# Kernel tuning notes

Measured on AMD Instinct MI355X. Metric: run time of the kernel, lower is better.

## Reference

```python
import jax, jax.numpy as jnp
import numpy as np

B, F, T, V, L, ATTR, E, H = 256, 2048, 40, 10000, 20, 400, 512, 1024
A = E            # attention_dim = embedding_dim
D1 = H + F + E   # lstm1 input dim
D2 = H + F       # lstm2 input dim


def setup_inputs() -> dict:
    key = jax.random.key(0)
    ks = jax.random.split(key, 16)
    def rn(k, shape, s=0.02):
        return jax.random.normal(k, shape, jnp.float32) * s
    return dict(
        input_feats=jax.random.normal(ks[0], (B, F, T), jnp.float32),
        input_atts=jax.random.uniform(ks[1], (B, ATTR), jnp.float32),
        input_sents=jax.random.randint(ks[2], (B, L), 0, V),
        attr_W=rn(ks[3], (D2, ATTR)), attr_b=jnp.zeros((D2,), jnp.float32),
        emb=rn(ks[4], (V, E)),
        l1_Wih=rn(ks[5], (4 * H, D1)), l1_Whh=rn(ks[6], (4 * H, H)),
        l1_bih=jnp.zeros((4 * H,), jnp.float32), l1_bhh=jnp.zeros((4 * H,), jnp.float32),
        l2_Wih=rn(ks[7], (4 * H, D2)), l2_Whh=rn(ks[8], (4 * H, H)),
        l2_bih=jnp.zeros((4 * H,), jnp.float32), l2_bhh=jnp.zeros((4 * H,), jnp.float32),
        prob_W=rn(ks[9], (V, H)), prob_b=jnp.zeros((V,), jnp.float32),
        attf_W=rn(ks[10], (A, F)), attf_b=jnp.zeros((A,), jnp.float32),
        atth_W=rn(ks[11], (A, H)), atth_b=jnp.zeros((A,), jnp.float32),
        atta_W=rn(ks[12], (1, A)), atta_b=jnp.zeros((1,), jnp.float32),
    )


def lstm_cell(x, h, c, Wih, Whh, bih, bhh):
    # torch.nn.LSTMCell gate order: i, f, g, o
    g = x @ Wih.T + bih + h @ Whh.T + bhh
    i, f, gg, o = jnp.split(g, 4, axis=1)
    c_new = jax.nn.sigmoid(f) * c + jax.nn.sigmoid(i) * jnp.tanh(gg)
    h_new = jax.nn.sigmoid(o) * jnp.tanh(c_new)
    return h_new, c_new


def reference(input_feats, input_atts, input_sents, attr_W, attr_b, emb,
              l1_Wih, l1_Whh, l1_bih, l1_bhh, l2_Wih, l2_Whh, l2_bih, l2_bhh,
              prob_W, prob_b, attf_W, attf_b, atth_W, atth_b, atta_W, atta_b):
    mean_feature = input_feats.mean(axis=2)                       # [B,F]
    # attention_linear_f(features) is timestep-independent: precompute once
    embed_f = jnp.einsum('bft,af->bta', input_feats, attf_W) + attf_b  # [B,T,A]

    zeros = jnp.zeros((B, H), jnp.float32)
    h1, c1 = zeros, zeros
    # lstm2 primed with embedded attributes
    attr_vec = input_atts @ attr_W.T + attr_b                     # [B,D2]
    h2, c2 = lstm_cell(attr_vec, zeros, zeros, l2_Wih, l2_Whh, l2_bih, l2_bhh)

    word_vecs = emb[input_sents[:, :L - 1]]                       # [B,L-1,E] teacher forcing

    def step(carry, wv):
        h1, c1, h2, c2 = carry
        x1 = jnp.concatenate([h2, mean_feature, wv], axis=1)      # [B,D1]
        h1, c1 = lstm_cell(x1, h1, c1, l1_Wih, l1_Whh, l1_bih, l1_bhh)
        # soft attention over T feature slots
        eh = h1 @ atth_W.T + atth_b                               # [B,A]
        scores = jnp.tanh(embed_f + eh[:, None, :]) @ atta_W[0] + atta_b[0]  # [B,T]
        alpha = jax.nn.softmax(scores, axis=1)                    # [B,T]
        v_hat = jnp.einsum('bt,bft->bf', alpha, input_feats)      # [B,F]
        x2 = jnp.concatenate([h1, v_hat], axis=1)                 # [B,D2]
        h2, c2 = lstm_cell(x2, h2, c2, l2_Wih, l2_Whh, l2_bih, l2_bhh)
        predict = h2 @ prob_W.T + prob_b                          # [B,V]
        gen_word = jnp.argmax(predict, axis=1)                    # argmax(log_softmax) == argmax(logits)
        return (h1, c1, h2, c2), (gen_word, predict)

    _, (gens, preds) = jax.lax.scan(step, (h1, c1, h2, c2),
                                    jnp.swapaxes(word_vecs, 0, 1))
    outputs = gens.T                                              # [B,L-1]
    output_preds = jnp.swapaxes(preds, 0, 1)                      # [B,L-1,V]
    return outputs, output_preds
```

## Files before the change

kernel.cpp:

```cpp
#include <hip/hip_runtime.h>
#include <cmath>

#define B_ 256
#define F_ 2048
#define T_ 40
#define V_ 10000
#define L_ 20
#define ATTR_ 400
#define E_ 512
#define H_ 1024
#define A_ 512
#define NS_ 19

typedef float f32x4 __attribute__((ext_vector_type(4)));
typedef short bf16x8 __attribute__((ext_vector_type(8)));

__device__ __forceinline__ float sigm(float x) { return 1.0f / (1.0f + expf(-x)); }

__device__ __forceinline__ unsigned short f2bf(float x) {
    unsigned int u = __float_as_uint(x);
    u += 0x7fffu + ((u >> 16) & 1u);
    return (unsigned short)(u >> 16);
}
__device__ __forceinline__ float bf2f(unsigned short h) {
    return __uint_as_float(((unsigned int)h) << 16);
}
__device__ __forceinline__ void gload16(const void* g, void* l) {
    __builtin_amdgcn_global_load_lds(
        (const __attribute__((address_space(1))) unsigned int*)g,
        (__attribute__((address_space(3))) unsigned int*)l, 16, 0, 0);
}
__device__ __forceinline__ f32x4 mfma16(bf16x8 a, bf16x8 b, f32x4 c) {
    return __builtin_amdgcn_mfma_f32_16x16x32_bf16(a, b, c, 0, 0, 0);
}
__device__ __forceinline__ long swz(int m, int k, int mslabs) {
    return ((long)(k >> 5) * mslabs + (m >> 4)) * 512
         + ((k >> 3) & 3) * 128 + (m & 15) * 8 + (k & 7);
}

struct GChunk {
    const unsigned short* Ahi; const unsigned short* Alo;
    const unsigned short* Bhi; const unsigned short* Blo;
    long ask, bsk;
    int kc;
};
struct GChunks { GChunk c[8]; };

template<int DIRECT>
__global__ __launch_bounds__(512) void gemm_mfma(
    GChunks ch, float* __restrict__ out, const float* __restrict__ bias,
    int Mreal, long ldc, long zstride)
{
    const GChunk cc = ch.c[blockIdx.z];
    const int tid  = threadIdx.x;
    const int lane = tid & 63;
    const int w    = tid >> 6;
    const int m0   = blockIdx.x * 128;
    const int n0   = blockIdx.y * 256;

    __shared__ __align__(16) unsigned short lds[3][48][512];

    const unsigned short* gp[6];
    long adv[6];
#pragma unroll
    for (int q = 0; q < 6; ++q) {
        int s = w * 6 + q;
        const unsigned short* base; long off;
        if (s < 16) {
            base = (s & 8) ? cc.Alo : cc.Ahi;
            off = ((long)(m0 >> 4) + (s & 7)) * 512;
            adv[q] = cc.ask;
        } else {
            int t2 = s - 16;
            base = (t2 & 16) ? cc.Blo : cc.Bhi;
            off = ((long)(n0 >> 4) + (t2 & 15)) * 512;
            adv[q] = cc.bsk;
        }
        gp[q] = base + off + lane * 8;
    }

    auto stage = [&](int t) {
#pragma unroll
        for (int q = 0; q < 6; ++q) {
            gload16(gp[q], &lds[t][w * 6 + q][lane * 8]);
            gp[q] += adv[q];
        }
    };

    f32x4 zero4 = {0.f, 0.f, 0.f, 0.f};
    f32x4 acc[4][4];
#pragma unroll
    for (int i = 0; i < 4; ++i)
#pragma unroll
        for (int j = 0; j < 4; ++j) acc[i][j] = zero4;

    const int ms0 = (w >> 2) * 4;
    const int ns0 = (w & 3) * 4;

    const int kst = cc.kc >> 5;
    stage(0);
    if (kst > 1) stage(1);
    for (int ks = 0; ks < kst; ++ks) {
        if (ks + 1 < kst) asm volatile("s_waitcnt vmcnt(6)" ::: "memory");
        else              asm volatile("s_waitcnt vmcnt(0)" ::: "memory");
        __builtin_amdgcn_s_barrier();
        __builtin_amdgcn_sched_barrier(0);
        if (ks + 2 < kst) stage((ks + 2) % 3);
        const unsigned short (*buf)[512] = lds[ks % 3];
        bf16x8 ah[4], al[4], bh[4], bl[4];
#pragma unroll
        for (int i = 0; i < 4; ++i) {
            ah[i] = *(const bf16x8*)&buf[ms0 + i][lane * 8];
            al[i] = *(const bf16x8*)&buf[8 + ms0 + i][lane * 8];
            bh[i] = *(const bf16x8*)&buf[16 + ns0 + i][lane * 8];
            bl[i] = *(const bf16x8*)&buf[32 + ns0 + i][lane * 8];
        }
#pragma unroll
        for (int i = 0; i < 4; ++i)
#pragma unroll
            for (int j = 0; j < 4; ++j) {
                acc[i][j] = mfma16(ah[i], bh[j], acc[i][j]);
                acc[i][j] = mfma16(ah[i], bl[j], acc[i][j]);
                acc[i][j] = mfma16(al[i], bh[j], acc[i][j]);
            }
    }

    const int wm = (w >> 2) * 64;
    const int wn = (w & 3) * 64;
    const int mr = (lane >> 4) * 4;
    const int ncl = lane & 15;
    float* P = DIRECT ? out : out + (long)blockIdx.z * zstride;
#pragma unroll
    for (int i = 0; i < 4; ++i) {
        int mm = m0 + wm + i * 16 + mr;
        if (mm < Mreal) {
            float4 bv = {0.f, 0.f, 0.f, 0.f};
            if (DIRECT && bias) bv = *(const float4*)&bias[mm];
#pragma unroll
            for (int j = 0; j < 4; ++j) {
                int bb = n0 + wn + j * 16 + ncl;
                float4 v;
                v.x = acc[i][j].x + bv.x;
                v.y = acc[i][j].y + bv.y;
                v.z = acc[i][j].z + bv.z;
                v.w = acc[i][j].w + bv.w;
                *(float4*)&P[(long)bb * ldc + mm] = v;
            }
        }
    }
}

__global__ __launch_bounds__(256) void lstm_fused(
    const float* __restrict__ P, int nz, long zstride,
    const float* __restrict__ base, int bmode,
    float* __restrict__ c,
    unsigned short* __restrict__ hhi, unsigned short* __restrict__ hlo)
{
    int idx = blockIdx.x * 256 + threadIdx.x;
    int n = idx & 1023;
    int b = idx >> 10;
    long r = (long)b * 4096 + n;
    float ig = 0.f, fg = 0.f, gg = 0.f, og = 0.f;
    for (int z = 0; z < nz; ++z) {
        const float* p = P + (long)z * zstride + r;
        ig += p[0]; fg += p[1024]; gg += p[2048]; og += p[3072];
    }
    if (bmode == 1) {
        const float* q = base + r;
        ig += q[0]; fg += q[1024]; gg += q[2048]; og += q[3072];
    } else {
        ig += base[n]; fg += base[1024 + n]; gg += base[2048 + n]; og += base[3072 + n];
    }
    float cn = sigm(fg) * c[idx] + sigm(ig) * tanhf(gg);
    c[idx] = cn;
    float hv = sigm(og) * tanhf(cn);
    unsigned short hi = f2bf(hv);
    long o = swz(b, n, 16);
    hhi[o] = hi;
    hlo[o] = f2bf(hv - bf2f(hi));
}

__global__ __launch_bounds__(256) void attention_kernel(
    const float* __restrict__ ef, const float* __restrict__ Pe,
    const float* __restrict__ feats, const float* __restrict__ atta_W,
    const float* __restrict__ atta_b,
    unsigned short* __restrict__ vhhi, unsigned short* __restrict__ vhlo)
{
    __shared__ float eh_s[512], aw_s[512], sc_s[48];
    int b = blockIdx.x, tid = threadIdx.x;
    float e0 = 0.f, e1 = 0.f;
#pragma unroll
    for (int z = 0; z < 8; ++z) {
        const float* p = Pe + (long)z * (512 * 256) + b * 512;
        e0 += p[tid]; e1 += p[tid + 256];
    }
    eh_s[tid] = e0; eh_s[tid + 256] = e1;
    aw_s[tid] = atta_W[tid]; aw_s[tid + 256] = atta_W[tid + 256];
    __syncthreads();
    int w = tid >> 6, lane = tid & 63;
    float ab0 = atta_b[0];
    for (int i = 0; i < 10; ++i) {
        int t = w * 10 + i;
        const float* ep = ef + ((long)b * T_ + t) * A_ + lane * 8;
        float4 e1v = *(const float4*)ep;
        float4 e2v = *(const float4*)(ep + 4);
        int a = lane * 8;
        float s = tanhf(e1v.x + eh_s[a+0]) * aw_s[a+0] + tanhf(e1v.y + eh_s[a+1]) * aw_s[a+1]
                + tanhf(e1v.z + eh_s[a+2]) * aw_s[a+2] + tanhf(e1v.w + eh_s[a+3]) * aw_s[a+3]
                + tanhf(e2v.x + eh_s[a+4]) * aw_s[a+4] + tanhf(e2v.y + eh_s[a+5]) * aw_s[a+5]
                + tanhf(e2v.z + eh_s[a+6]) * aw_s[a+6] + tanhf(e2v.w + eh_s[a+7]) * aw_s[a+7];
#pragma unroll
        for (int o = 32; o > 0; o >>= 1) s += __shfl_down(s, o, 64);
        if (lane == 0) sc_s[t] = s + ab0;
    }
    __syncthreads();
    if (tid < 64) {
        float v = (tid < T_) ? sc_s[tid] : -INFINITY;
        float m = v;
#pragma unroll
        for (int o = 32; o > 0; o >>= 1) m = fmaxf(m, __shfl_down(m, o, 64));
        m = __shfl(m, 0, 64);
        float e = (tid < T_) ? expf(v - m) : 0.f;
        float su = e;
#pragma unroll
        for (int o = 32; o > 0; o >>= 1) su += __shfl_down(su, o, 64);
        su = __shfl(su, 0, 64);
        if (tid < T_) sc_s[tid] = e / su;
    }
    __syncthreads();
    for (int cc = 0; cc < 8; ++cc) {
        int f = cc * 256 + tid;
        const float* fp = feats + ((long)b * F_ + f) * T_;
        float acc = 0.f;
#pragma unroll
        for (int t4 = 0; t4 < 10; ++t4) {
            float4 v = *(const float4*)(fp + t4 * 4);
            acc += sc_s[t4*4+0] * v.x + sc_s[t4*4+1] * v.y
                 + sc_s[t4*4+2] * v.z + sc_s[t4*4+3] * v.w;
        }
        unsigned short hi = f2bf(acc);
        long o = swz(b, f, 16);
        vhhi[o] = hi;
        vhlo[o] = f2bf(acc - bf2f(hi));
    }
}

__global__ void reduce_rows(float* __restrict__ out, const float* __restrict__ P,
                            const float* __restrict__ base, int S, long zstride,
                            int n, int mask)
{
    long e = ((long)blockIdx.x * 256 + threadIdx.x) * 4;
    if (e >= n) return;
    float4 s = *(const float4*)&P[e];
    for (int z = 1; z < S; ++z) {
        float4 p = *(const float4*)&P[(long)z * zstride + e];
        s.x += p.x; s.y += p.y; s.z += p.z; s.w += p.w;
    }
    if (base) {
        float4 bv = *(const float4*)&base[e & mask];
        s.x += bv.x; s.y += bv.y; s.z += bv.z; s.w += bv.w;
    }
    *(float4*)&out[e] = s;
}

__global__ void cast_swz(const float* __restrict__ src,
    unsigned short* __restrict__ dhi, unsigned short* __restrict__ dlo,
    long srcld, int nrows, int ncols, int mslabs)
{
    long g = (long)blockIdx.x * 256 + threadIdx.x;
    int within = (int)(g & 511);
    long slab = g >> 9;
    int kblk = (int)(slab / mslabs);
    int ms = (int)(slab - (long)kblk * mslabs);
    int kg = within >> 7, r = (within >> 3) & 15, j = within & 7;
    int m = ms * 16 + r;
    int k = kblk * 32 + kg * 8 + j;
    float v = (m < nrows && k < ncols) ? src[(long)m * srcld + k] : 0.f;
    unsigned short hi = f2bf(v);
    dhi[g] = hi; dlo[g] = f2bf(v - bf2f(hi));
}

__global__ void mean_cast(const float* __restrict__ feats,
                          unsigned short* __restrict__ mh, unsigned short* __restrict__ ml)
{
    int idx = blockIdx.x * 256 + threadIdx.x;
    const float* p = feats + (long)idx * T_;
    float s = 0.f;
#pragma unroll
    for (int t = 0; t < T_; t += 4) {
        float4 v = *(const float4*)(p + t);
        s += v.x + v.y + v.z + v.w;
    }
    s *= (1.0f / (float)T_);
    unsigned short hi = f2bf(s);
    int b = idx >> 11, f = idx & 2047;
    long o = swz(b, f, 16);
    mh[o] = hi; ml[o] = f2bf(s - bf2f(hi));
}

__global__ __launch_bounds__(256) void transpose_cast_feats(
    const float* __restrict__ feats,
    unsigned short* __restrict__ fh, unsigned short* __restrict__ fl)
{
    __shared__ float tf[2560];
    int b = blockIdx.y, f0 = blockIdx.x * 64;
    const float* src = feats + (long)b * (F_ * T_) + (long)f0 * T_;
#pragma unroll
    for (int q = 0; q < 10; ++q) tf[q * 256 + threadIdx.x] = src[q * 256 + threadIdx.x];
    __syncthreads();
#pragma unroll
    for (int q = 0; q < 10; ++q) {
        int idx = q * 256 + threadIdx.x;
        int t = idx >> 6, fo = idx & 63;
        int f = f0 + fo;
        int bt = b * T_ + t;
        float v = tf[fo * 40 + t];
        unsigned short hi = f2bf(v);
        long o = ((long)(f >> 5) * 640 + (bt >> 4)) * 512
               + ((f >> 3) & 3) * 128 + (bt & 15) * 8 + (f & 7);
        fh[o] = hi; fl[o] = f2bf(v - bf2f(hi));
    }
}

__global__ void wv_gather_cast(const int* __restrict__ sents, const float* __restrict__ emb,
    unsigned short* __restrict__ wh, unsigned short* __restrict__ wl, int s)
{
    int idx = blockIdx.x * 256 + threadIdx.x;
    int b = idx >> 9, e = idx & 511;
    int wd = sents[b * L_ + s];
    float v = emb[(long)wd * E_ + e];
    unsigned short hi = f2bf(v);
    long o = swz(b, e, 16);
    wh[o] = hi; wl[o] = f2bf(v - bf2f(hi));
}

__global__ void vec_add_kernel(const float* a, const float* b, float* out, int n)
{
    int i = blockIdx.x * 256 + threadIdx.x;
    if (i < n) out[i] = a[i] + b[i];
}

__global__ __launch_bounds__(256) void argmax_kernel(
    const float* __restrict__ dout_preds, float* __restrict__ outw, int s)
{
    __shared__ float sv[256];
    __shared__ int   si[256];
    int b = blockIdx.x, tid = threadIdx.x;
    const float* row = dout_preds + (long)b * (NS_ * (long)V_) + (long)s * V_;
    float best = -INFINITY; int bi = 0x7fffffff;
    for (int v = tid; v < V_; v += 256) {
        float x = row[v];
        if (x > best) { best = x; bi = v; }
    }
    sv[tid] = best; si[tid] = bi;
    __syncthreads();
    for (int o = 128; o > 0; o >>= 1) {
        if (tid < o) {
            float ov = sv[tid + o]; int oi = si[tid + o];
            if (ov > sv[tid] || (ov == sv[tid] && oi < si[tid])) { sv[tid] = ov; si[tid] = oi; }
        }
        __syncthreads();
    }
    if (tid == 0) outw[b * NS_ + s] = (float)si[0];
}

extern "C" void kernel_launch(void* const* d_in, const int* in_sizes, int n_in,
                              void* d_out, int out_size, void* d_ws, size_t ws_size,
                              hipStream_t stream)
{
    (void)in_sizes; (void)n_in; (void)out_size; (void)ws_size;
    const float* feats  = (const float*)d_in[0];
    const float* atts   = (const float*)d_in[1];
    const int*   sents  = (const int*)d_in[2];
    const float* attr_W = (const float*)d_in[3];
    const float* attr_b = (const float*)d_in[4];
    const float* emb    = (const float*)d_in[5];
    const float* l1_Wih = (const float*)d_in[6];
    const float* l1_Whh = (const float*)d_in[7];
    const float* l1_bih = (const float*)d_in[8];
    const float* l1_bhh = (const float*)d_in[9];
    const float* l2_Wih = (const float*)d_in[10];
    const float* l2_Whh = (const float*)d_in[11];
    const float* l2_bih = (const float*)d_in[12];
    const float* l2_bhh = (const float*)d_in[13];
    const float* prob_W = (const float*)d_in[14];
    const float* prob_b = (const float*)d_in[15];
    const float* attf_W = (const float*)d_in[16];
    const float* attf_b = (const float*)d_in[17];
    const float* atth_W = (const float*)d_in[18];
    const float* atth_b = (const float*)d_in[19];
    const float* atta_W = (const float*)d_in[20];
    const float* atta_b = (const float*)d_in[21];

    float* out = (float*)d_out;
    float* preds = out + B_ * NS_;

    char* pp = (char*)d_ws;
    auto alloc = [&](size_t n) { char* r = pp; pp += (n + 255) & ~(size_t)255; return r; };

    const long AS256 = 256L * 512;
    const long AS632 = 632L * 512;
    const long AS32  = 32L * 512;
    const long AS192 = 192L * 512;
    const long BS    = 16L * 512;
    const long BS640 = 640L * 512;

    char* R = alloc(83886080UL);
    unsigned short* fTh   = (unsigned short*)R;
    unsigned short* fTl   = (unsigned short*)(R + 41943040UL);
    unsigned short* W2ihh = (unsigned short*)R;
    unsigned short* W2ihl = (unsigned short*)(R + 25165824UL);
    unsigned short* Wmh   = (unsigned short*)(R + 50331648UL);
    unsigned short* Wml   = (unsigned short*)(R + 67108864UL);

    unsigned short* W1ah  = (unsigned short*)alloc(8388608);
    unsigned short* W1al  = (unsigned short*)alloc(8388608);
    unsigned short* W1wh  = (unsigned short*)alloc(4194304);
    unsigned short* W1wl  = (unsigned short*)alloc(4194304);
    unsigned short* W1hhh = (unsigned short*)alloc(8388608);
    unsigned short* W1hhl = (unsigned short*)alloc(8388608);
    unsigned short* W2hhh = (unsigned short*)alloc(8388608);
    unsigned short* W2hhl = (unsigned short*)alloc(8388608);
    unsigned short* Wprh  = (unsigned short*)alloc(20709376);
    unsigned short* Wprl  = (unsigned short*)alloc(20709376);
    unsigned short* Wahh  = (unsigned short*)alloc(1048576);
    unsigned short* Wahl  = (unsigned short*)alloc(1048576);
    unsigned short* Wafh  = (unsigned short*)alloc(2097152);
    unsigned short* Wafl  = (unsigned short*)alloc(2097152);
    unsigned short* Warh  = (unsigned short*)alloc(2555904);
    unsigned short* Warl  = (unsigned short*)alloc(2555904);

    float* ef    = (float*)alloc(10240L*512*4);
    float* base1 = (float*)alloc(4096L*256*4);
    float* Pbuf  = (float*)alloc(7L*4096*256*4);
    float* attrv = Pbuf;

    unsigned short* h1h = (unsigned short*)alloc(524288);
    unsigned short* h1l = (unsigned short*)alloc(524288);
    unsigned short* h2h = (unsigned short*)alloc(524288);
    unsigned short* h2l = (unsigned short*)alloc(524288);
    unsigned short* wvh = (unsigned short*)alloc(262144);
    unsigned short* wvl = (unsigned short*)alloc(262144);
    unsigned short* vhh = (unsigned short*)alloc(1048576);
    unsigned short* vhl = (unsigned short*)alloc(1048576);
    unsigned short* mfh = (unsigned short*)alloc(1048576);
    unsigned short* mfl = (unsigned short*)alloc(1048576);
    unsigned short* attsh = (unsigned short*)alloc(212992);
    unsigned short* attsl = (unsigned short*)alloc(212992);
    unsigned short* avh = (unsigned short*)alloc(1572864);
    unsigned short* avl = (unsigned short*)alloc(1572864);
    float* c1 = (float*)alloc(256L*1024*4);
    float* c2 = (float*)alloc(256L*1024*4);
    float* bihbhh1 = (float*)alloc(4096*4);
    float* bias2   = (float*)alloc(4096*4);
    float* efbias  = (float*)alloc(512*4);

    hipMemsetAsync(c1, 0, 256L*1024*4, stream);
    hipMemsetAsync(c2, 0, 256L*1024*4, stream);
    hipMemsetAsync(h1h, 0, 524288, stream);
    hipMemsetAsync(h1l, 0, 524288, stream);

    vec_add_kernel<<<16, 256, 0, stream>>>(l1_bih, l1_bhh, bihbhh1, 4096);
    vec_add_kernel<<<16, 256, 0, stream>>>(l2_bih, l2_bhh, bias2, 4096);
    vec_add_kernel<<<2, 256, 0, stream>>>(attf_b, atth_b, efbias, 512);
    mean_cast<<<2048, 256, 0, stream>>>(feats, mfh, mfl);

    cast_swz<<<16384, 256, 0, stream>>>(l1_Wih,        W1ah, W1al, 3584, 4096, 1024, 256);
    cast_swz<<< 8192, 256, 0, stream>>>(l1_Wih + 3072, W1wh, W1wl, 3584, 4096,  512, 256);
    cast_swz<<<16384, 256, 0, stream>>>(l1_Whh, W1hhh, W1hhl, 1024, 4096, 1024, 256);
    cast_swz<<<16384, 256, 0, stream>>>(l2_Whh, W2hhh, W2hhl, 1024, 4096, 1024, 256);
    cast_swz<<<40448, 256, 0, stream>>>(prob_W, Wprh, Wprl, 1024, 10000, 1024, 632);
    cast_swz<<< 2048, 256, 0, stream>>>(atth_W, Wahh, Wahl, 1024, 512, 1024, 32);
    cast_swz<<< 4096, 256, 0, stream>>>(attf_W, Wafh, Wafl, 2048, 512, 2048, 32);
    cast_swz<<< 4992, 256, 0, stream>>>(attr_W, Warh, Warl, 400, 3072, 400, 192);
    cast_swz<<<  416, 256, 0, stream>>>(atts,   attsh, attsl, 400, 256, 400, 16);

    transpose_cast_feats<<<dim3(32,256), 256, 0, stream>>>(feats, fTh, fTl);
    {
        GChunks ch = {};
        ch.c[0] = {Wafh, Wafl, fTh, fTl, AS32, BS640, 2048};
        gemm_mfma<1><<<dim3(4,40,1), 512, 0, stream>>>(ch, ef, efbias, 512, 512L, 0);
    }
    {
        GChunks ch = {};
        ch.c[0] = {Warh, Warl, attsh, attsl, AS192, BS, 416};
        gemm_mfma<1><<<dim3(24,1,1), 512, 0, stream>>>(ch, attrv, attr_b, 3072, 3072L, 0);
        cast_swz<<<3072, 256, 0, stream>>>(attrv, avh, avl, 3072, 256, 3072, 16);
    }
    cast_swz<<<49152, 256, 0, stream>>>(l2_Wih,        W2ihh, W2ihl, 3072, 4096, 3072, 256);
    cast_swz<<<32768, 256, 0, stream>>>(l1_Wih + 1024, Wmh,   Wml,   3584, 4096, 2048, 256);
    {
        GChunks ch = {};
        for (int z = 0; z < 2; ++z)
            ch.c[z] = {Wmh + z*32*AS256, Wml + z*32*AS256,
                       mfh + z*32*BS,    mfl + z*32*BS, AS256, BS, 1024};
        gemm_mfma<0><<<dim3(32,1,2), 512, 0, stream>>>(ch, Pbuf, nullptr, 4096, 4096L, 4096L*256);
        reduce_rows<<<1024, 256, 0, stream>>>(base1, Pbuf, bihbhh1, 2, 4096L*256, 4096*256, 4095);
    }
    {
        GChunks ch = {};
        for (int z = 0; z < 3; ++z)
            ch.c[z] = {W2ihh + z*32*AS256, W2ihl + z*32*AS256,
                       avh + z*32*BS,      avl + z*32*BS, AS256, BS, 1024};
        gemm_mfma<0><<<dim3(32,1,3), 512, 0, stream>>>(ch, Pbuf, nullptr, 4096, 4096L, 4096L*256);
        lstm_fused<<<1024, 256, 0, stream>>>(Pbuf, 3, 4096L*256, bias2, 2, c2, h2h, h2l);
    }

    GChunks chG1 = {};
    chG1.c[0] = {W1ah,              W1al,              h2h,          h2l,          AS256, BS, 512};
    chG1.c[1] = {W1ah + 16*AS256,   W1al + 16*AS256,   h2h + 16*BS,  h2l + 16*BS,  AS256, BS, 512};
    chG1.c[2] = {W1wh,              W1wl,              wvh,          wvl,          AS256, BS, 512};
    chG1.c[3] = {W1hhh,             W1hhl,             h1h,          h1l,          AS256, BS, 512};
    chG1.c[4] = {W1hhh + 16*AS256,  W1hhl + 16*AS256,  h1h + 16*BS,  h1l + 16*BS,  AS256, BS, 512};
    GChunks chEh = {};
    for (int z = 0; z < 8; ++z)
        chEh.c[z] = {Wahh + z*4*AS32, Wahl + z*4*AS32,
                     h1h + z*4*BS,    h1l + z*4*BS, AS32, BS, 128};
    GChunks chG2 = {};
    chG2.c[0] = {W2ihh,             W2ihl,             h1h,          h1l,          AS256, BS, 512};
    chG2.c[1] = {W2ihh + 16*AS256,  W2ihl + 16*AS256,  h1h + 16*BS,  h1l + 16*BS,  AS256, BS, 512};
    chG2.c[2] = {W2ihh + 32*AS256,  W2ihl + 32*AS256,  vhh,          vhl,          AS256, BS, 512};
    chG2.c[3] = {W2ihh + 48*AS256,  W2ihl + 48*AS256,  vhh + 16*BS,  vhl + 16*BS,  AS256, BS, 512};
    chG2.c[4] = {W2ihh + 64*AS256,  W2ihl + 64*AS256,  vhh + 32*BS,  vhl + 32*BS,  AS256, BS, 1024};
    chG2.c[5] = {W2hhh,             W2hhl,             h2h,          h2l,          AS256, BS, 512};
    chG2.c[6] = {W2hhh + 16*AS256,  W2hhl + 16*AS256,  h2h + 16*BS,  h2l + 16*BS,  AS256, BS, 512};
    GChunks chPr = {};
    chPr.c[0] = {Wprh, Wprl, h2h, h2l, AS632, BS, 1024};

    for (int s = 0; s < NS_; ++s) {
        wv_gather_cast<<<512, 256, 0, stream>>>(sents, emb, wvh, wvl, s);

        gemm_mfma<0><<<dim3(32,1,5), 512, 0, stream>>>(chG1, Pbuf, nullptr, 4096, 4096L, 4096L*256);
        lstm_fused<<<1024, 256, 0, stream>>>(Pbuf, 5, 4096L*256, base1, 1, c1, h1h, h1l);

        gemm_mfma<0><<<dim3(4,1,8), 512, 0, stream>>>(chEh, Pbuf, nullptr, 512, 512L, 512L*256);
        attention_kernel<<<256, 256, 0, stream>>>(ef, Pbuf, feats, atta_W, atta_b, vhh, vhl);

        gemm_mfma<0><<<dim3(32,1,7), 512, 0, stream>>>(chG2, Pbuf, nullptr, 4096, 4096L, 4096L*256);
        lstm_fused<<<1024, 256, 0, stream>>>(Pbuf, 7, 4096L*256, bias2, 2, c2, h2h, h2l);

        gemm_mfma<1><<<dim3(79,1,1), 512, 0, stream>>>(
            chPr, preds + (long)s * V_, prob_b, 10000, (long)NS_ * V_, 0);

        argmax_kernel<<<256, 256, 0, stream>>>(preds, out, s);
    }
}
```

Baseline: 4.553 ms.

## Merge per-step GEMMs into ragged chunk launches and defer projection/argmax across steps

Makes the GEMM kernel chunk-indexed along the x dimension, so that chunks with different outputs, bias, K and M can share one grid. Per step it fuses the layer1 GEMMs, the layer2 h-recurrent GEMM and the previous step's vocab projection into one launch. The previous step's argmax is folded into the layer1 LSTM kernel as extra blocks, and all word-embedding gathers are hoisted into one launch before the loop. This cuts launch count and serialization and raises occupancy per launch, at the cost of more workspace and more complex chunk bookkeeping.

```diff
diff --git a/kernel.cpp b/kernel.cpp
--- a/kernel.cpp
+++ b/kernel.cpp
@@ -41,21 +41,23 @@
 struct GChunk {
     const unsigned short* Ahi; const unsigned short* Alo;
     const unsigned short* Bhi; const unsigned short* Blo;
-    long ask, bsk;
-    int kc;
+    float* out; const float* bias;
+    long ask, bsk, ldc;
+    int kc, x0, Mreal;
 };
 struct GChunks { GChunk c[8]; };
 
-template<int DIRECT>
-__global__ __launch_bounds__(512) void gemm_mfma(
-    GChunks ch, float* __restrict__ out, const float* __restrict__ bias,
-    int Mreal, long ldc, long zstride)
-{
-    const GChunk cc = ch.c[blockIdx.z];
+__global__ __launch_bounds__(512) void gemm_mfma(GChunks ch)
+{
+    const int bx = blockIdx.x;
+    int ci = 0;
+#pragma unroll
+    for (int i = 1; i < 8; ++i) if (ch.c[i].x0 <= bx) ci = i;
+    const GChunk cc = ch.c[ci];
     const int tid  = threadIdx.x;
     const int lane = tid & 63;
     const int w    = tid >> 6;
-    const int m0   = blockIdx.x * 128;
+    const int m0   = (bx - cc.x0) * 128;
     const int n0   = blockIdx.y * 256;
 
     __shared__ __align__(16) unsigned short lds[3][48][512];
@@ -129,13 +131,13 @@
     const int wn = (w & 3) * 64;
     const int mr = (lane >> 4) * 4;
     const int ncl = lane & 15;
-    float* P = DIRECT ? out : out + (long)blockIdx.z * zstride;
+    float* P = cc.out;
 #pragma unroll
     for (int i = 0; i < 4; ++i) {
         int mm = m0 + wm + i * 16 + mr;
-        if (mm < Mreal) {
+        if (mm < cc.Mreal) {
             float4 bv = {0.f, 0.f, 0.f, 0.f};
-            if (DIRECT && bias) bv = *(const float4*)&bias[mm];
+            if (cc.bias) bv = *(const float4*)&cc.bias[mm];
 #pragma unroll
             for (int j = 0; j < 4; ++j) {
                 int bb = n0 + wn + j * 16 + ncl;
@@ -144,7 +146,7 @@
                 v.y = acc[i][j].y + bv.y;
                 v.z = acc[i][j].z + bv.z;
                 v.w = acc[i][j].w + bv.w;
-                *(float4*)&P[(long)bb * ldc + mm] = v;
+                *(float4*)&P[(long)bb * cc.ldc + mm] = v;
             }
         }
     }
@@ -154,8 +156,31 @@
     const float* __restrict__ P, int nz, long zstride,
     const float* __restrict__ base, int bmode,
     float* __restrict__ c,
-    unsigned short* __restrict__ hhi, unsigned short* __restrict__ hlo)
-{
+    unsigned short* __restrict__ hhi, unsigned short* __restrict__ hlo,
+    const float* __restrict__ preds_all, float* __restrict__ outw, int sarg)
+{
+    if (blockIdx.x >= 1024) {
+        __shared__ float sv[256];
+        __shared__ int   si[256];
+        int b = blockIdx.x - 1024, tid = threadIdx.x;
+        const float* row = preds_all + (long)b * (NS_ * (long)V_) + (long)sarg * V_;
+        float best = -INFINITY; int bi = 0x7fffffff;
+        for (int v = tid; v < V_; v += 256) {
+            float x = row[v];
+            if (x > best) { best = x; bi = v; }
+        }
+        sv[tid] = best; si[tid] = bi;
+        __syncthreads();
+        for (int o = 128; o > 0; o >>= 1) {
+            if (tid < o) {
+                float ov = sv[tid + o]; int oi = si[tid + o];
+                if (ov > sv[tid] || (ov == sv[tid] && oi < si[tid])) { sv[tid] = ov; si[tid] = oi; }
+            }
+            __syncthreads();
+        }
+        if (tid == 0) outw[b * NS_ + sarg] = (float)si[0];
+        return;
+    }
     int idx = blockIdx.x * 256 + threadIdx.x;
     int n = idx & 1023;
     int b = idx >> 10;
@@ -322,15 +347,17 @@
     }
 }
 
-__global__ void wv_gather_cast(const int* __restrict__ sents, const float* __restrict__ emb,
-    unsigned short* __restrict__ wh, unsigned short* __restrict__ wl, int s)
+__global__ void wv_gather_cast_all(const int* __restrict__ sents,
+    const float* __restrict__ emb,
+    unsigned short* __restrict__ wh, unsigned short* __restrict__ wl)
 {
     int idx = blockIdx.x * 256 + threadIdx.x;
+    int s = blockIdx.y;
     int b = idx >> 9, e = idx & 511;
     int wd = sents[b * L_ + s];
     float v = emb[(long)wd * E_ + e];
     unsigned short hi = f2bf(v);
-    long o = swz(b, e, 16);
+    long o = (long)s * 131072 + swz(b, e, 16);
     wh[o] = hi; wl[o] = f2bf(v - bf2f(hi));
 }
 
@@ -404,6 +431,7 @@
     const long AS192 = 192L * 512;
     const long BS    = 16L * 512;
     const long BS640 = 640L * 512;
+    const long SLOT  = 4096L * 256;
 
     char* R = alloc(83886080UL);
     unsigned short* fTh   = (unsigned short*)R;
@@ -432,15 +460,16 @@
 
     float* ef    = (float*)alloc(10240L*512*4);
     float* base1 = (float*)alloc(4096L*256*4);
-    float* Pbuf  = (float*)alloc(7L*4096*256*4);
+    float* Pbuf  = (float*)alloc(10L*4096*256*4);
+    float* ehP   = (float*)alloc(8L*512*256*4);
     float* attrv = Pbuf;
 
     unsigned short* h1h = (unsigned short*)alloc(524288);
     unsigned short* h1l = (unsigned short*)alloc(524288);
     unsigned short* h2h = (unsigned short*)alloc(524288);
     unsigned short* h2l = (unsigned short*)alloc(524288);
-    unsigned short* wvh = (unsigned short*)alloc(262144);
-    unsigned short* wvl = (unsigned short*)alloc(262144);
+    unsigned short* wvh = (unsigned short*)alloc(19L*131072*2);
+    unsigned short* wvl = (unsigned short*)alloc(19L*131072*2);
     unsigned short* vhh = (unsigned short*)alloc(1048576);
     unsigned short* vhl = (unsigned short*)alloc(1048576);
     unsigned short* mfh = (unsigned short*)alloc(1048576);
@@ -455,6 +484,10 @@
     float* bias2   = (float*)alloc(4096*4);
     float* efbias  = (float*)alloc(512*4);
 
+    auto seal = [](GChunks& g, int used) {
+        for (int i = used; i < 8; ++i) g.c[i].x0 = 0x7fffffff;
+    };
+
     hipMemsetAsync(c1, 0, 256L*1024*4, stream);
     hipMemsetAsync(c2, 0, 256L*1024*4, stream);
     hipMemsetAsync(h1h, 0, 524288, stream);
@@ -464,6 +497,7 @@
     vec_add_kernel<<<16, 256, 0, stream>>>(l2_bih, l2_bhh, bias2, 4096);
     vec_add_kernel<<<2, 256, 0, stream>>>(attf_b, atth_b, efbias, 512);
     mean_cast<<<2048, 256, 0, stream>>>(feats, mfh, mfl);
+    wv_gather_cast_all<<<dim3(512, 19), 256, 0, stream>>>(sents, emb, wvh, wvl);
 
     cast_swz<<<16384, 256, 0, stream>>>(l1_Wih,        W1ah, W1al, 3584, 4096, 1024, 256);
     cast_swz<<< 8192, 256, 0, stream>>>(l1_Wih + 3072, W1wh, W1wl, 3584, 4096,  512, 256);
@@ -477,71 +511,84 @@
 
     transpose_cast_feats<<<dim3(32,256), 256, 0, stream>>>(feats, fTh, fTl);
     {
-        GChunks ch = {};
-        ch.c[0] = {Wafh, Wafl, fTh, fTl, AS32, BS640, 2048};
-        gemm_mfma<1><<<dim3(4,40,1), 512, 0, stream>>>(ch, ef, efbias, 512, 512L, 0);
+        GChunks g = {};
+        g.c[0] = {Wafh, Wafl, fTh, fTl, ef, efbias, AS32, BS640, 512L, 2048, 0, 512};
+        seal(g, 1);
+        gemm_mfma<<<dim3(4,40), 512, 0, stream>>>(g);
     }
     {
-        GChunks ch = {};
-        ch.c[0] = {Warh, Warl, attsh, attsl, AS192, BS, 416};
-        gemm_mfma<1><<<dim3(24,1,1), 512, 0, stream>>>(ch, attrv, attr_b, 3072, 3072L, 0);
+        GChunks g = {};
+        g.c[0] = {Warh, Warl, attsh, attsl, attrv, attr_b, AS192, BS, 3072L, 416, 0, 3072};
+        seal(g, 1);
+        gemm_mfma<<<dim3(24,1), 512, 0, stream>>>(g);
         cast_swz<<<3072, 256, 0, stream>>>(attrv, avh, avl, 3072, 256, 3072, 16);
     }
     cast_swz<<<49152, 256, 0, stream>>>(l2_Wih,        W2ihh, W2ihl, 3072, 4096, 3072, 256);
     cast_swz<<<32768, 256, 0, stream>>>(l1_Wih + 1024, Wmh,   Wml,   3584, 4096, 2048, 256);
     {
-        GChunks ch = {};
-        for (int z = 0; z < 2; ++z)
-            ch.c[z] = {Wmh + z*32*AS256, Wml + z*32*AS256,
-                       mfh + z*32*BS,    mfl + z*32*BS, AS256, BS, 1024};
-        gemm_mfma<0><<<dim3(32,1,2), 512, 0, stream>>>(ch, Pbuf, nullptr, 4096, 4096L, 4096L*256);
-        reduce_rows<<<1024, 256, 0, stream>>>(base1, Pbuf, bihbhh1, 2, 4096L*256, 4096*256, 4095);
+        GChunks g = {};
+        g.c[0] = {Wmh,           Wml,           mfh,        mfl,        Pbuf,        nullptr, AS256, BS, 4096L, 1024,  0, 4096};
+        g.c[1] = {Wmh+32*AS256,  Wml+32*AS256,  mfh+32*BS,  mfl+32*BS,  Pbuf+SLOT,   nullptr, AS256, BS, 4096L, 1024, 32, 4096};
+        seal(g, 2);
+        gemm_mfma<<<dim3(64,1), 512, 0, stream>>>(g);
+        reduce_rows<<<1024, 256, 0, stream>>>(base1, Pbuf, bihbhh1, 2, SLOT, 4096*256, 4095);
     }
     {
-        GChunks ch = {};
+        GChunks g = {};
         for (int z = 0; z < 3; ++z)
-            ch.c[z] = {W2ihh + z*32*AS256, W2ihl + z*32*AS256,
-                       avh + z*32*BS,      avl + z*32*BS, AS256, BS, 1024};
-        gemm_mfma<0><<<dim3(32,1,3), 512, 0, stream>>>(ch, Pbuf, nullptr, 4096, 4096L, 4096L*256);
-        lstm_fused<<<1024, 256, 0, stream>>>(Pbuf, 3, 4096L*256, bias2, 2, c2, h2h, h2l);
-    }
-
-    GChunks chG1 = {};
-    chG1.c[0] = {W1ah,              W1al,              h2h,          h2l,          AS256, BS, 512};
-    chG1.c[1] = {W1ah + 16*AS256,   W1al + 16*AS256,   h2h + 16*BS,  h2l + 16*BS,  AS256, BS, 512};
-    chG1.c[2] = {W1wh,              W1wl,              wvh,          wvl,          AS256, BS, 512};
-    chG1.c[3] = {W1hhh,             W1hhl,             h1h,          h1l,          AS256, BS, 512};
-    chG1.c[4] = {W1hhh + 16*AS256,  W1hhl + 16*AS256,  h1h + 16*BS,  h1l + 16*BS,  AS256, BS, 512};
-    GChunks chEh = {};
+            g.c[z] = {W2ihh+z*32*AS256, W2ihl+z*32*AS256, avh+z*32*BS, avl+z*32*BS,
+                      Pbuf+z*SLOT, nullptr, AS256, BS, 4096L, 1024, z*32, 4096};
+        seal(g, 3);
+        gemm_mfma<<<dim3(96,1), 512, 0, stream>>>(g);
+        lstm_fused<<<1024, 256, 0, stream>>>(Pbuf, 3, SLOT, bias2, 2, c2, h2h, h2l,
+                                             nullptr, nullptr, -1);
+    }
+
+    GChunks gEh = {};
     for (int z = 0; z < 8; ++z)
-        chEh.c[z] = {Wahh + z*4*AS32, Wahl + z*4*AS32,
-                     h1h + z*4*BS,    h1l + z*4*BS, AS32, BS, 128};
-    GChunks chG2 = {};
-    chG2.c[0] = {W2ihh,             W2ihl,             h1h,          h1l,          AS256, BS, 512};
-    chG2.c[1] = {W2ihh + 16*AS256,  W2ihl + 16*AS256,  h1h + 16*BS,  h1l + 16*BS,  AS256, BS, 512};
-    chG2.c[2] = {W2ihh + 32*AS256,  W2ihl + 32*AS256,  vhh,          vhl,          AS256, BS, 512};
-    chG2.c[3] = {W2ihh + 48*AS256,  W2ihl + 48*AS256,  vhh + 16*BS,  vhl + 16*BS,  AS256, BS, 512};
-    chG2.c[4] = {W2ihh + 64*AS256,  W2ihl + 64*AS256,  vhh + 32*BS,  vhl + 32*BS,  AS256, BS, 1024};
-    chG2.c[5] = {W2hhh,             W2hhl,             h2h,          h2l,          AS256, BS, 512};
-    chG2.c[6] = {W2hhh + 16*AS256,  W2hhl + 16*AS256,  h2h + 16*BS,  h2l + 16*BS,  AS256, BS, 512};
-    GChunks chPr = {};
-    chPr.c[0] = {Wprh, Wprl, h2h, h2l, AS632, BS, 1024};
+        gEh.c[z] = {Wahh+z*4*AS32, Wahl+z*4*AS32, h1h+z*4*BS, h1l+z*4*BS,
+                    ehP + (long)z*512*256, nullptr, AS32, BS, 512L, 128, z*4, 512};
+    GChunks gG2 = {};
+    {
+        const unsigned short* Bh[6] = {h1h, h1h+16*BS, vhh, vhh+16*BS, vhh+32*BS, vhh+48*BS};
+        const unsigned short* Bl[6] = {h1l, h1l+16*BS, vhl, vhl+16*BS, vhl+32*BS, vhl+48*BS};
+        for (int q = 0; q < 6; ++q)
+            gG2.c[q] = {W2ihh+q*16*AS256, W2ihl+q*16*AS256, Bh[q], Bl[q],
+                        Pbuf+(4+q)*SLOT, nullptr, AS256, BS, 4096L, 512, q*32, 4096};
+        seal(gG2, 6);
+    }
 
     for (int s = 0; s < NS_; ++s) {
-        wv_gather_cast<<<512, 256, 0, stream>>>(sents, emb, wvh, wvl, s);
-
-        gemm_mfma<0><<<dim3(32,1,5), 512, 0, stream>>>(chG1, Pbuf, nullptr, 4096, 4096L, 4096L*256);
-        lstm_fused<<<1024, 256, 0, stream>>>(Pbuf, 5, 4096L*256, base1, 1, c1, h1h, h1l);
-
-        gemm_mfma<0><<<dim3(4,1,8), 512, 0, stream>>>(chEh, Pbuf, nullptr, 512, 512L, 512L*256);
-        attention_kernel<<<256, 256, 0, stream>>>(ef, Pbuf, feats, atta_W, atta_b, vhh, vhl);
-
-        gemm_mfma<0><<<dim3(32,1,7), 512, 0, stream>>>(chG2, Pbuf, nullptr, 4096, 4096L, 4096L*256);
-        lstm_fused<<<1024, 256, 0, stream>>>(Pbuf, 7, 4096L*256, bias2, 2, c2, h2h, h2l);
-
-        gemm_mfma<1><<<dim3(79,1,1), 512, 0, stream>>>(
-            chPr, preds + (long)s * V_, prob_b, 10000, (long)NS_ * V_, 0);
-
-        argmax_kernel<<<256, 256, 0, stream>>>(preds, out, s);
-    }
-}
+        GChunks g1 = {};
+        g1.c[0] = {W1ah,  W1al,  h2h, h2l, Pbuf,        nullptr, AS256, BS, 4096L, 1024,  0, 4096};
+        g1.c[1] = {W1wh,  W1wl,  wvh + (long)s*131072, wvl + (long)s*131072,
+                   Pbuf+SLOT,   nullptr, AS256, BS, 4096L,  512, 32, 4096};
+        g1.c[2] = {W1hhh, W1hhl, h1h, h1l, Pbuf+2*SLOT, nullptr, AS256, BS, 4096L, 1024, 64, 4096};
+        g1.c[3] = {W2hhh, W2hhl, h2h, h2l, Pbuf+3*SLOT, nullptr, AS256, BS, 4096L, 1024, 96, 4096};
+        int nblk = 128;
+        if (s > 0) {
+            g1.c[4] = {Wprh, Wprl, h2h, h2l, preds + (long)(s-1)*V_, prob_b,
+                       AS632, BS, (long)NS_*V_, 1024, 128, 10000};
+            nblk = 207; seal(g1, 5);
+        } else seal(g1, 4);
+        gemm_mfma<<<dim3(nblk,1), 512, 0, stream>>>(g1);
+
+        lstm_fused<<<(s > 0 ? 1280 : 1024), 256, 0, stream>>>(
+            Pbuf, 3, SLOT, base1, 1, c1, h1h, h1l, preds, out, s - 1);
+
+        gemm_mfma<<<dim3(32,1), 512, 0, stream>>>(gEh);
+        attention_kernel<<<256, 256, 0, stream>>>(ef, ehP, feats, atta_W, atta_b, vhh, vhl);
+
+        gemm_mfma<<<dim3(192,1), 512, 0, stream>>>(gG2);
+        lstm_fused<<<1024, 256, 0, stream>>>(Pbuf + 3*SLOT, 7, SLOT, bias2, 2, c2, h2h, h2l,
+                                             nullptr, nullptr, -1);
+    }
+    {
+        GChunks g = {};
+        g.c[0] = {Wprh, Wprl, h2h, h2l, preds + 18L*V_, prob_b,
+                  AS632, BS, (long)NS_*V_, 1024, 0, 10000};
+        seal(g, 1);
+        gemm_mfma<<<dim3(79,1), 512, 0, stream>>>(g);
+        argmax_kernel<<<256, 256, 0, stream>>>(preds, out, 18);
+    }
+}
```

Result: faster. 3.723 ms (-18.2%).
